# Performance work log

Hardware: AMD Instinct MI355X
Metric: run time of the kernel (lower is better)

Reference implementation:

```python
import jax, jax.numpy as jnp
import numpy as np

D_MODEL = 1024
N_HEAD = 16
HEAD_D = D_MODEL // N_HEAD
D_FF = 4096
LN_EPS = 1e-5
ATTN_EPS = 1e-6


def _layer_norm(x, g, b, eps=LN_EPS):
    mu = jnp.mean(x, axis=-1, keepdims=True)
    var = jnp.var(x, axis=-1, keepdims=True)
    return (x - mu) * jax.lax.rsqrt(var + eps) * g + b


def setup_inputs() -> dict:
    key = jax.random.key(0)
    ks = jax.random.split(key, 16)
    s = 0.02
    return {
        "src": jax.random.normal(ks[0], (4, 4096, D_MODEL), dtype=jnp.float32),
        "qkv_w": jax.random.normal(ks[1], (D_MODEL, 3 * D_MODEL), dtype=jnp.float32) * s,
        "qkv_b": jax.random.normal(ks[2], (3 * D_MODEL,), dtype=jnp.float32) * s,
        "out_w": jax.random.normal(ks[3], (D_MODEL, D_MODEL), dtype=jnp.float32) * s,
        "out_b": jax.random.normal(ks[4], (D_MODEL,), dtype=jnp.float32) * s,
        "w1": jax.random.normal(ks[5], (D_MODEL, D_FF), dtype=jnp.float32) * s,
        "b1": jax.random.normal(ks[6], (D_FF,), dtype=jnp.float32) * s,
        "w2": jax.random.normal(ks[7], (D_FF, D_MODEL), dtype=jnp.float32) * s,
        "b2": jax.random.normal(ks[8], (D_MODEL,), dtype=jnp.float32) * s,
        "g1": jnp.ones((D_MODEL,), dtype=jnp.float32),
        "be1": jnp.zeros((D_MODEL,), dtype=jnp.float32),
        "g2": jnp.ones((D_MODEL,), dtype=jnp.float32),
        "be2": jnp.zeros((D_MODEL,), dtype=jnp.float32),
    }


def _linear_attention(x, qkv_w, qkv_b, out_w, out_b):
    B, N, C = x.shape
    qkv = (x @ qkv_w + qkv_b).reshape(B, N, 3, N_HEAD, HEAD_D)
    qkv = jnp.transpose(qkv, (2, 0, 3, 1, 4))  # [3,B,H,N,D]
    q, k, v = qkv[0], qkv[1], qkv[2]
    # phi = elu(x) + 1 (positive feature map)
    qf = jax.nn.elu(q) + 1.0
    kf = jax.nn.elu(k) + 1.0
    # kv aggregation: [B,H,D,D]
    kv = jnp.einsum('bhnd,bhne->bhde', kf.astype(jnp.float32), v.astype(jnp.float32)).astype(v.dtype)
    y_num = jnp.einsum('bhnd,bhde->bhne', qf, kv)  # [B,H,N,D]
    z = jnp.sum(kf.astype(jnp.float32), axis=2)  # [B,H,D]
    y_den = jnp.einsum('bhnd,bhd->bhn', qf, z.astype(qf.dtype))
    y_den = jnp.maximum(y_den, ATTN_EPS)[..., None]
    y = (y_num / y_den).transpose(0, 2, 1, 3).reshape(B, N, C)
    return y @ out_w + out_b


def reference(src, qkv_w, qkv_b, out_w, out_b, w1, b1, w2, b2, g1, be1, g2, be2):
    # pre-norm (norm_first=True), dropout disabled (eval)
    attn_out = _linear_attention(_layer_norm(src, g1, be1), qkv_w, qkv_b, out_w, out_b)
    x = src + attn_out
    h = jax.nn.gelu(_layer_norm(x, g2, be2) @ w1 + b1, approximate=False)
    return x + h @ w2 + b2
```

## Files before the change

### kernel.cpp

```cpp
#include <hip/hip_runtime.h>
#include <hip/hip_bf16.h>
#include <math.h>

typedef __attribute__((ext_vector_type(8))) short short8;
typedef __attribute__((ext_vector_type(4))) float floatx4;

__device__ __forceinline__ float bf2f(unsigned int u) {
    union { unsigned int i; float f; } c; c.i = u << 16; return c.f;
}
__device__ __forceinline__ unsigned short f2bf(float f) {
    unsigned int x = __builtin_bit_cast(unsigned int, f);
    unsigned int r = (x + 0x7fffu + ((x >> 16) & 1u)) >> 16;
    return (unsigned short)r;
}
__device__ __forceinline__ float elu1(float x) { return x > 0.f ? x + 1.f : __expf(x); }
__device__ __forceinline__ float gelu_exact(float x) {
    return 0.5f * x * (1.f + erff(x * 0.70710678118654752f));
}

__device__ __forceinline__ void async_cp16(const void* g, void* l) {
    __builtin_amdgcn_global_load_lds(
        (const __attribute__((address_space(1))) unsigned int*)g,
        (__attribute__((address_space(3))) unsigned int*)l, 16, 0, 0);
}

__global__ void prep_kernel(const float* __restrict__ qkv_w, const float* __restrict__ out_w,
                            const float* __restrict__ w1, const float* __restrict__ w2,
                            unsigned short* __restrict__ qkvwT, unsigned short* __restrict__ outwT,
                            unsigned short* __restrict__ w1T, unsigned short* __restrict__ w2T,
                            float* __restrict__ kvz) {
    const int bid = blockIdx.x;
    const int tx = threadIdx.x, ty = threadIdx.y;
    if (bid >= 12288) {
        const int lid = ty * 32 + tx;
        const int i = (bid - 12288) * 1024 + lid * 4;
        *(float4*)(kvz + i) = make_float4(0.f, 0.f, 0.f, 0.f);
        return;
    }
    const float* in;
    unsigned short* op;
    int K, N, tb;
    if (bid < 3072)      { in = qkv_w; op = qkvwT; K = 1024; N = 3072; tb = bid; }
    else if (bid < 4096) { in = out_w; op = outwT; K = 1024; N = 1024; tb = bid - 3072; }
    else if (bid < 8192) { in = w1;    op = w1T;   K = 1024; N = 4096; tb = bid - 4096; }
    else                 { in = w2;    op = w2T;   K = 4096; N = 1024; tb = bid - 8192; }
    const int nx = N >> 5;
    const int n0 = (tb % nx) * 32, k0 = (tb / nx) * 32;
    __shared__ float tile[32][33];
#pragma unroll
    for (int i = 0; i < 4; i++)
        tile[ty + 8 * i][tx] = in[(size_t)(k0 + ty + 8 * i) * N + n0 + tx];
    __syncthreads();
#pragma unroll
    for (int i = 0; i < 4; i++)
        op[(size_t)(n0 + ty + 8 * i) * K + k0 + tx] = f2bf(tile[tx][ty + 8 * i]);
}

__global__ __launch_bounds__(256)
void ln_kernel(const float* __restrict__ x, const float* __restrict__ g,
               const float* __restrict__ be, unsigned short* __restrict__ out) {
    const int row = blockIdx.x;
    const int t = threadIdx.x;
    const float4 v = *(const float4*)(x + (size_t)row * 1024 + t * 4);
    float s = v.x + v.y + v.z + v.w;
    float s2 = v.x * v.x + v.y * v.y + v.z * v.z + v.w * v.w;
#pragma unroll
    for (int off = 32; off > 0; off >>= 1) {
        s += __shfl_down(s, off);
        s2 += __shfl_down(s2, off);
    }
    __shared__ float red[8];
    __shared__ float stat[2];
    const int w = t >> 6, l = t & 63;
    if (l == 0) { red[w] = s; red[4 + w] = s2; }
    __syncthreads();
    if (t == 0) {
        float S = red[0] + red[1] + red[2] + red[3];
        float S2 = red[4] + red[5] + red[6] + red[7];
        float mu = S * (1.f / 1024.f);
        float var = S2 * (1.f / 1024.f) - mu * mu;
        stat[0] = mu;
        stat[1] = rsqrtf(var + 1e-5f);
    }
    __syncthreads();
    const float mu = stat[0], rs = stat[1];
    const float4 gv = *(const float4*)(g + t * 4);
    const float4 bv = *(const float4*)(be + t * 4);
    unsigned int o0 = f2bf((v.x - mu) * rs * gv.x + bv.x);
    unsigned int o1 = f2bf((v.y - mu) * rs * gv.y + bv.y);
    unsigned int o2 = f2bf((v.z - mu) * rs * gv.z + bv.z);
    unsigned int o3 = f2bf((v.w - mu) * rs * gv.w + bv.w);
    uint2 pk;
    pk.x = o0 | (o1 << 16);
    pk.y = o2 | (o3 << 16);
    *(uint2*)(out + (size_t)row * 1024 + t * 4) = pk;
}

template <int EPI>
__global__ __launch_bounds__(256, 4)
void gemm_bt(const unsigned short* __restrict__ A, const unsigned short* __restrict__ B,
             const float* __restrict__ bias, const float* __restrict__ resid,
             unsigned short* __restrict__ Cbf, float* __restrict__ Cf32,
             int N, int K) {
    __shared__ unsigned short At[128 * 32];
    __shared__ unsigned short Bt[128 * 32];
    const int t = threadIdx.x;
    const int l = t & 63;
    const int w = t >> 6;

    const int T = gridDim.x * gridDim.y;
    const int f = blockIdx.y * gridDim.x + blockIdx.x;
    int bx = blockIdx.x, by = blockIdx.y;
    if ((T & 7) == 0) {
        const int per = T >> 3;
        const int g = (f & 7) * per + (f >> 3);
        bx = g % gridDim.x;
        by = g / gridDim.x;
    }
    const int m0 = by * 128;
    const int n0 = bx * 128;
    const int wm = (w >> 1) * 64;
    const int wn = (w & 1) * 64;

    floatx4 acc[4][4];
    const floatx4 zz = {0.f, 0.f, 0.f, 0.f};
#pragma unroll
    for (int i = 0; i < 4; i++)
#pragma unroll
        for (int j = 0; j < 4; j++) acc[i][j] = zz;

    const int sr = t >> 2;
    const int sc = (t & 3) << 3;
    const unsigned short* ag = A + (size_t)(m0 + sr) * K + sc;
    const unsigned short* ag2 = ag + (size_t)64 * K;
    const unsigned short* bg = B + (size_t)(n0 + sr) * K + sc;
    const unsigned short* bg2 = bg + (size_t)64 * K;
    unsigned short* la = At + t * 8;
    unsigned short* la2 = At + 2048 + t * 8;
    unsigned short* lb = Bt + t * 8;
    unsigned short* lb2 = Bt + 2048 + t * 8;

    const int fr = l & 15;
    const int fo = (l >> 4) << 3;

    for (int k0 = 0; k0 < K; k0 += 32) {
        async_cp16(ag + k0, la);
        async_cp16(ag2 + k0, la2);
        async_cp16(bg + k0, lb);
        async_cp16(bg2 + k0, lb2);
        __syncthreads();
        short8 af[4], bf[4];
#pragma unroll
        for (int i = 0; i < 4; i++)
            af[i] = *(const short8*)(At + (wm + i * 16 + fr) * 32 + fo);
#pragma unroll
        for (int i = 0; i < 4; i++)
            bf[i] = *(const short8*)(Bt + (wn + i * 16 + fr) * 32 + fo);
#pragma unroll
        for (int i = 0; i < 4; i++)
#pragma unroll
            for (int j = 0; j < 4; j++)
                acc[i][j] = __builtin_amdgcn_mfma_f32_16x16x32_bf16(af[i], bf[j], acc[i][j], 0, 0, 0);
        __syncthreads();
    }

    const int er = (l >> 4) << 2;
    const int ec = l & 15;
#pragma unroll
    for (int j = 0; j < 4; j++) {
        const int col = n0 + wn + j * 16 + ec;
        const float bb = bias[col];
#pragma unroll
        for (int i = 0; i < 4; i++) {
            const int rowb = m0 + wm + i * 16 + er;
#pragma unroll
            for (int r = 0; r < 4; r++) {
                const int row = rowb + r;
                float v = acc[i][j][r] + bb;
                const size_t idx = (size_t)row * N + col;
                if (EPI == 0) {
                    if (col < 2048) v = elu1(v);
                    Cbf[idx] = f2bf(v);
                } else if (EPI == 1) {
                    Cf32[idx] = v + resid[idx];
                } else {
                    Cbf[idx] = f2bf(gelu_exact(v));
                }
            }
        }
    }
}

__global__ __launch_bounds__(256)
void kv_kernel(const unsigned short* __restrict__ qkv, float* __restrict__ kvz) {
    const int bh = blockIdx.x;
    const int chunk = blockIdx.y;
    const int b = bh >> 4, h = bh & 15;
    const int t = threadIdx.x;
    __shared__ float kf[64][68];
    __shared__ float vv[64][68];
    const int te = t >> 4, td = t & 15;
    float acc[4][4];
#pragma unroll
    for (int i = 0; i < 4; i++)
#pragma unroll
        for (int j = 0; j < 4; j++) acc[i][j] = 0.f;
    float zacc = 0.f;
    const size_t base = (size_t)b * 4096 * 3072 + (size_t)chunk * 512 * 3072;
    const int koff = 1024 + h * 64;
    const int voff = 2048 + h * 64;
    const int rl = t >> 3, seg = t & 7;

    for (int s = 0; s < 8; s++) {
#pragma unroll
        for (int p = 0; p < 2; p++) {
            const int nl = p * 32 + rl;
            const unsigned short* rp = qkv + base + (size_t)(s * 64 + nl) * 3072;
            const uint4 kd = *(const uint4*)(rp + koff + seg * 8);
            const uint4 vd = *(const uint4*)(rp + voff + seg * 8);
            float* kdst = &kf[nl][seg * 8];
            float* vdst = &vv[nl][seg * 8];
            kdst[0] = bf2f(kd.x & 0xffff); kdst[1] = bf2f(kd.x >> 16);
            kdst[2] = bf2f(kd.y & 0xffff); kdst[3] = bf2f(kd.y >> 16);
            kdst[4] = bf2f(kd.z & 0xffff); kdst[5] = bf2f(kd.z >> 16);
            kdst[6] = bf2f(kd.w & 0xffff); kdst[7] = bf2f(kd.w >> 16);
            vdst[0] = bf2f(vd.x & 0xffff); vdst[1] = bf2f(vd.x >> 16);
            vdst[2] = bf2f(vd.y & 0xffff); vdst[3] = bf2f(vd.y >> 16);
            vdst[4] = bf2f(vd.z & 0xffff); vdst[5] = bf2f(vd.z >> 16);
            vdst[6] = bf2f(vd.w & 0xffff); vdst[7] = bf2f(vd.w >> 16);
        }
        __syncthreads();
        for (int n = 0; n < 64; n++) {
            const float4 kk = *(const float4*)&kf[n][te * 4];
            const float4 vn = *(const float4*)&vv[n][td * 4];
            const float ka[4] = {kk.x, kk.y, kk.z, kk.w};
            const float va[4] = {vn.x, vn.y, vn.z, vn.w};
#pragma unroll
            for (int i = 0; i < 4; i++)
#pragma unroll
                for (int j = 0; j < 4; j++) acc[i][j] = fmaf(ka[i], va[j], acc[i][j]);
        }
        if (t < 64) {
            for (int n = 0; n < 64; n++) zacc += kf[n][t];
        }
        __syncthreads();
    }
    float* kvp = kvz + bh * 4160;
#pragma unroll
    for (int i = 0; i < 4; i++)
#pragma unroll
        for (int j = 0; j < 4; j++)
            atomicAdd(&kvp[(te * 4 + i) * 64 + td * 4 + j], acc[i][j]);
    if (t < 64) atomicAdd(&kvp[4096 + t], zacc);
}

__global__ __launch_bounds__(256)
void y_kernel(const unsigned short* __restrict__ qkv, const float* __restrict__ kvz,
              unsigned short* __restrict__ y) {
    const int bh = blockIdx.x, chunk = blockIdx.y;
    const int b = bh >> 4, h = bh & 15;
    const int t = threadIdx.x;
    __shared__ float kv[64][68];
    __shared__ float zs[64];
    __shared__ float qf[16][68];
    const float* kvp = kvz + bh * 4160;
#pragma unroll
    for (int p = 0; p < 4; p++) {
        const int f = (t + p * 256) * 4;
        const float4 v4 = *(const float4*)(kvp + f);
        *(float4*)&kv[f >> 6][f & 63] = v4;
    }
    if (t < 16) *(float4*)&zs[t * 4] = *(const float4*)(kvp + 4096 + t * 4);
    __syncthreads();
    const int nl = t >> 4, td = t & 15;
    const size_t base = (size_t)b * 4096 * 3072 + (size_t)chunk * 128 * 3072;
    const int qoff = h * 64;
    for (int s = 0; s < 8; s++) {
        if (t < 128) {
            const int r = t >> 3, seg = t & 7;
            const uint4 qd = *(const uint4*)(qkv + base + (size_t)(s * 16 + r) * 3072 + qoff + seg * 8);
            float* qdst = &qf[r][seg * 8];
            qdst[0] = bf2f(qd.x & 0xffff); qdst[1] = bf2f(qd.x >> 16);
            qdst[2] = bf2f(qd.y & 0xffff); qdst[3] = bf2f(qd.y >> 16);
            qdst[4] = bf2f(qd.z & 0xffff); qdst[5] = bf2f(qd.z >> 16);
            qdst[6] = bf2f(qd.w & 0xffff); qdst[7] = bf2f(qd.w >> 16);
        }
        __syncthreads();
        float a0 = 0.f, a1 = 0.f, a2 = 0.f, a3 = 0.f, den = 0.f;
        for (int e = 0; e < 64; e++) {
            const float q = qf[nl][e];
            const float4 kvv = *(const float4*)&kv[e][td * 4];
            a0 = fmaf(q, kvv.x, a0);
            a1 = fmaf(q, kvv.y, a1);
            a2 = fmaf(q, kvv.z, a2);
            a3 = fmaf(q, kvv.w, a3);
            den = fmaf(q, zs[e], den);
        }
        const float inv = 1.f / fmaxf(den, 1e-6f);
        const int tok = b * 4096 + chunk * 128 + s * 16 + nl;
        unsigned int o0 = f2bf(a0 * inv), o1 = f2bf(a1 * inv);
        unsigned int o2 = f2bf(a2 * inv), o3 = f2bf(a3 * inv);
        uint2 pk;
        pk.x = o0 | (o1 << 16);
        pk.y = o2 | (o3 << 16);
        *(uint2*)(y + (size_t)tok * 1024 + h * 64 + td * 4) = pk;
        __syncthreads();
    }
}

extern "C" void kernel_launch(void* const* d_in, const int* in_sizes, int n_in,
                              void* d_out, int out_size, void* d_ws, size_t ws_size,
                              hipStream_t stream) {
    const float* src   = (const float*)d_in[0];
    const float* qkv_w = (const float*)d_in[1];
    const float* qkv_b = (const float*)d_in[2];
    const float* out_w = (const float*)d_in[3];
    const float* out_b = (const float*)d_in[4];
    const float* w1    = (const float*)d_in[5];
    const float* b1    = (const float*)d_in[6];
    const float* w2    = (const float*)d_in[7];
    const float* b2    = (const float*)d_in[8];
    const float* g1    = (const float*)d_in[9];
    const float* be1   = (const float*)d_in[10];
    const float* g2    = (const float*)d_in[11];
    const float* be2   = (const float*)d_in[12];
    float* outp = (float*)d_out;

    char* ws = (char*)d_ws;
    unsigned short* qkvwT = (unsigned short*)(ws + 0);
    unsigned short* outwT = (unsigned short*)(ws + 6291456);
    unsigned short* w1T   = (unsigned short*)(ws + 8388608);
    unsigned short* w2T   = (unsigned short*)(ws + 16777216);
    unsigned short* bufA  = (unsigned short*)(ws + 25165824);
    unsigned short* bufB  = (unsigned short*)(ws + 159383552);
    float*          xbuf  = (float*)(ws + 192937984);
    float*          kvz   = (float*)(ws + 260046848);

    prep_kernel<<<12548, dim3(32, 8), 0, stream>>>(qkv_w, out_w, w1, w2,
                                                   qkvwT, outwT, w1T, w2T, kvz);

    ln_kernel<<<16384, 256, 0, stream>>>(src, g1, be1, bufB);
    gemm_bt<0><<<dim3(24, 128), 256, 0, stream>>>(bufB, qkvwT, qkv_b, nullptr, bufA, nullptr, 3072, 1024);
    kv_kernel<<<dim3(64, 8), 256, 0, stream>>>(bufA, kvz);
    y_kernel<<<dim3(64, 32), 256, 0, stream>>>(bufA, kvz, bufB);
    gemm_bt<1><<<dim3(8, 128), 256, 0, stream>>>(bufB, outwT, out_b, src, nullptr, xbuf, 1024, 1024);
    ln_kernel<<<16384, 256, 0, stream>>>(xbuf, g2, be2, bufB);
    gemm_bt<2><<<dim3(32, 128), 256, 0, stream>>>(bufB, w1T, b1, nullptr, bufA, nullptr, 4096, 1024);
    gemm_bt<1><<<dim3(8, 128), 256, 0, stream>>>(bufA, w2T, b2, xbuf, nullptr, outp, 1024, 4096);
}
```

Measured before the change: 882.6 us.

## Swizzle GEMM LDS layout, store residual in bf16, use tanh-approx GELU

```diff
diff --git a/kernel.cpp b/kernel.cpp
--- a/kernel.cpp
+++ b/kernel.cpp
@@ -14,8 +14,9 @@
     return (unsigned short)r;
 }
 __device__ __forceinline__ float elu1(float x) { return x > 0.f ? x + 1.f : __expf(x); }
-__device__ __forceinline__ float gelu_exact(float x) {
-    return 0.5f * x * (1.f + erff(x * 0.70710678118654752f));
+__device__ __forceinline__ float gelu_fast(float x) {
+    float u = x * (1.f + 0.044715f * x * x);
+    return x / (1.f + __expf(-1.5957691216f * u));
 }
 
 __device__ __forceinline__ void async_cp16(const void* g, void* l) {
@@ -56,12 +57,21 @@
         op[(size_t)(n0 + ty + 8 * i) * K + k0 + tx] = f2bf(tile[tx][ty + 8 * i]);
 }
 
+template <int IN_BF16>
 __global__ __launch_bounds__(256)
-void ln_kernel(const float* __restrict__ x, const float* __restrict__ g,
+void ln_kernel(const void* __restrict__ xv, const float* __restrict__ g,
                const float* __restrict__ be, unsigned short* __restrict__ out) {
     const int row = blockIdx.x;
     const int t = threadIdx.x;
-    const float4 v = *(const float4*)(x + (size_t)row * 1024 + t * 4);
+    float4 v;
+    if (IN_BF16) {
+        const unsigned short* x = (const unsigned short*)xv;
+        uint2 r = *(const uint2*)(x + (size_t)row * 1024 + t * 4);
+        v.x = bf2f(r.x & 0xffff); v.y = bf2f(r.x >> 16);
+        v.z = bf2f(r.y & 0xffff); v.w = bf2f(r.y >> 16);
+    } else {
+        v = *(const float4*)((const float*)xv + (size_t)row * 1024 + t * 4);
+    }
     float s = v.x + v.y + v.z + v.w;
     float s2 = v.x * v.x + v.y * v.y + v.z * v.z + v.w * v.w;
 #pragma unroll
@@ -100,6 +110,7 @@
 __global__ __launch_bounds__(256, 4)
 void gemm_bt(const unsigned short* __restrict__ A, const unsigned short* __restrict__ B,
              const float* __restrict__ bias, const float* __restrict__ resid,
+             const unsigned short* __restrict__ residb,
              unsigned short* __restrict__ Cbf, float* __restrict__ Cf32,
              int N, int K) {
     __shared__ unsigned short At[128 * 32];
@@ -130,7 +141,7 @@
         for (int j = 0; j < 4; j++) acc[i][j] = zz;
 
     const int sr = t >> 2;
-    const int sc = (t & 3) << 3;
+    const int sc = (((t & 3) ^ ((t >> 3) & 3)) << 3);
     const unsigned short* ag = A + (size_t)(m0 + sr) * K + sc;
     const unsigned short* ag2 = ag + (size_t)64 * K;
     const unsigned short* bg = B + (size_t)(n0 + sr) * K + sc;
@@ -141,7 +152,7 @@
     unsigned short* lb2 = Bt + 2048 + t * 8;
 
     const int fr = l & 15;
-    const int fo = (l >> 4) << 3;
+    const int fo = (((l >> 4) ^ ((l >> 1) & 3)) << 3);
 
     for (int k0 = 0; k0 < K; k0 += 32) {
         async_cp16(ag + k0, la);
@@ -181,10 +192,12 @@
                 if (EPI == 0) {
                     if (col < 2048) v = elu1(v);
                     Cbf[idx] = f2bf(v);
-                } else if (EPI == 1) {
-                    Cf32[idx] = v + resid[idx];
+                } else if (EPI == 2) {
+                    Cbf[idx] = f2bf(gelu_fast(v));
+                } else if (EPI == 3) {
+                    Cbf[idx] = f2bf(v + resid[idx]);
                 } else {
-                    Cbf[idx] = f2bf(gelu_exact(v));
+                    Cf32[idx] = v + bf2f(residb[idx]);
                 }
             }
         }
@@ -333,18 +346,18 @@
     unsigned short* w2T   = (unsigned short*)(ws + 16777216);
     unsigned short* bufA  = (unsigned short*)(ws + 25165824);
     unsigned short* bufB  = (unsigned short*)(ws + 159383552);
-    float*          xbuf  = (float*)(ws + 192937984);
+    unsigned short* xbuf  = (unsigned short*)(ws + 192937984);
     float*          kvz   = (float*)(ws + 260046848);
 
     prep_kernel<<<12548, dim3(32, 8), 0, stream>>>(qkv_w, out_w, w1, w2,
                                                    qkvwT, outwT, w1T, w2T, kvz);
 
-    ln_kernel<<<16384, 256, 0, stream>>>(src, g1, be1, bufB);
-    gemm_bt<0><<<dim3(24, 128), 256, 0, stream>>>(bufB, qkvwT, qkv_b, nullptr, bufA, nullptr, 3072, 1024);
+    ln_kernel<0><<<16384, 256, 0, stream>>>(src, g1, be1, bufB);
+    gemm_bt<0><<<dim3(24, 128), 256, 0, stream>>>(bufB, qkvwT, qkv_b, nullptr, nullptr, bufA, nullptr, 3072, 1024);
     kv_kernel<<<dim3(64, 8), 256, 0, stream>>>(bufA, kvz);
     y_kernel<<<dim3(64, 32), 256, 0, stream>>>(bufA, kvz, bufB);
-    gemm_bt<1><<<dim3(8, 128), 256, 0, stream>>>(bufB, outwT, out_b, src, nullptr, xbuf, 1024, 1024);
-    ln_kernel<<<16384, 256, 0, stream>>>(xbuf, g2, be2, bufB);
-    gemm_bt<2><<<dim3(32, 128), 256, 0, stream>>>(bufB, w1T, b1, nullptr, bufA, nullptr, 4096, 1024);
-    gemm_bt<1><<<dim3(8, 128), 256, 0, stream>>>(bufA, w2T, b2, xbuf, nullptr, outp, 1024, 4096);
-}
+    gemm_bt<3><<<dim3(8, 128), 256, 0, stream>>>(bufB, outwT, out_b, src, nullptr, xbuf, nullptr, 1024, 1024);
+    ln_kernel<1><<<16384, 256, 0, stream>>>(xbuf, g2, be2, bufB);
+    gemm_bt<2><<<dim3(32, 128), 256, 0, stream>>>(bufB, w1T, b1, nullptr, nullptr, bufA, nullptr, 4096, 1024);
+    gemm_bt<4><<<dim3(8, 128), 256, 0, stream>>>(bufA, w2T, b2, nullptr, xbuf, nullptr, outp, 1024, 4096);
+}
```

New measurement: 847.0 us. -4.0%, faster.
